# Performance work log

Measured on AMD Instinct MI355X. Metric: run time of the kernel, lower is better.

Reference implementation:

```python
import jax, jax.numpy as jnp
import numpy as np

B, S, D = 2, 2048, 2048
H, KVH = 32, 8
HD = D // H            # 64
G = H // KVH           # 4 kv groups
SCALE = 1.0 / np.sqrt(HD)


def setup_inputs() -> dict:
    key = jax.random.key(0)
    k1, k2, k3, k4, k5 = jax.random.split(key, 5)
    hidden_states = jax.random.normal(k1, (B, S, D), dtype=jnp.float32)
    Wq = jax.random.normal(k2, (D, H * HD), dtype=jnp.float32) * 0.02
    Wk = jax.random.normal(k3, (D, KVH * HD), dtype=jnp.float32) * 0.02
    Wv = jax.random.normal(k4, (D, KVH * HD), dtype=jnp.float32) * 0.02
    Wo = jax.random.normal(k5, (H * HD, D), dtype=jnp.float32) * 0.02
    return {"hidden_states": hidden_states, "Wq": Wq, "Wk": Wk, "Wv": Wv, "Wo": Wo}


def reference(hidden_states, Wq, Wk, Wv, Wo):
    B_, S_, _ = hidden_states.shape
    q = (hidden_states @ Wq).reshape(B_, S_, H, HD).transpose(0, 2, 1, 3)      # [B,H,S,HD]
    k = (hidden_states @ Wk).reshape(B_, S_, KVH, HD).transpose(0, 2, 1, 3)    # [B,KVH,S,HD]
    v = (hidden_states @ Wv).reshape(B_, S_, KVH, HD).transpose(0, 2, 1, 3)
    # repeat_interleave over head dim: kv head g serves q heads [g*G, (g+1)*G)
    k = jnp.repeat(k, G, axis=1)  # [B,H,S,HD]
    v = jnp.repeat(v, G, axis=1)
    scores = jnp.einsum('bhqd,bhkd->bhqk', q, k) * SCALE
    probs = jax.nn.softmax(scores.astype(jnp.float32), axis=-1).astype(q.dtype)
    # dropout is identity in eval mode
    out = jnp.einsum('bhqk,bhkd->bhqd', probs, v)             # [B,H,S,HD]
    out = out.transpose(0, 2, 1, 3).reshape(B_, S_, H * HD)   # [B,S,D]
    return out @ Wo
```

## Files before the change

kernel.cpp:

```cpp
#include <hip/hip_runtime.h>
#include <hip/hip_bf16.h>

typedef unsigned short u16;
typedef __attribute__((ext_vector_type(8))) short short8;
typedef __attribute__((ext_vector_type(4))) float f32x4;
typedef __attribute__((ext_vector_type(4))) unsigned short u16x4;

#define S_LEN 2048
#define NH 32
#define NKV 8
#define QSCALE 0.18033688011112042f
#define PSHIFT 14.0f

__device__ __forceinline__ float fexp2(float x) { return __builtin_amdgcn_exp2f(x); }

__device__ __forceinline__ u16 f2bf(float f) {
  unsigned int u = __builtin_bit_cast(unsigned int, f);
  u += 0x7fffu + ((u >> 16) & 1u);
  return (u16)(u >> 16);
}

__device__ __forceinline__ unsigned int pk2bf(float a, float b) {
  float2 t; t.x = a; t.y = b;
  __hip_bfloat162 h = __float22bfloat162_rn(t);
  unsigned int r;
  __builtin_memcpy(&r, &h, 4);
  return r;
}

__device__ __forceinline__ void async16(const void* g, void* l) {
  __builtin_amdgcn_global_load_lds(
      (__attribute__((address_space(1))) void*)g,
      (__attribute__((address_space(3))) void*)l, 16, 0, 0);
}

__global__ __launch_bounds__(256) void prep_kernel(const float* __restrict__ X,
                                                   const float* __restrict__ Wq,
                                                   const float* __restrict__ Wk,
                                                   const float* __restrict__ Wv,
                                                   const float* __restrict__ Wo,
                                                   u16* __restrict__ Xb,
                                                   u16* __restrict__ Wqt,
                                                   u16* __restrict__ Wkt,
                                                   u16* __restrict__ Wvt,
                                                   u16* __restrict__ Wot) {
  __shared__ float tile[32][33];
  int bx = blockIdx.x, tid = threadIdx.x;
  if (bx < 8192) {
    int idx = bx * 256 + tid;
    float4 v = ((const float4*)X)[idx];
    u16x4 o;
    o.x = f2bf(v.x); o.y = f2bf(v.y); o.z = f2bf(v.z); o.w = f2bf(v.w);
    *(u16x4*)&Xb[(size_t)idx * 4] = o;
    return;
  }
  const float* in; u16* out; int N, bi;
  if (bx < 12288)      { bi = bx - 8192;  in = Wq; out = Wqt; N = 2048; }
  else if (bx < 13312) { bi = bx - 12288; in = Wk; out = Wkt; N = 512; }
  else if (bx < 14336) { bi = bx - 13312; in = Wv; out = Wvt; N = 512; }
  else                 { bi = bx - 14336; in = Wo; out = Wot; N = 2048; }
  const int K = 2048;
  int nbx = N >> 5;
  int n0 = (bi % nbx) * 32, k0 = (bi / nbx) * 32;
  int tx = tid & 31, ty = tid >> 5;
#pragma unroll
  for (int i = 0; i < 32; i += 8)
    tile[ty + i][tx] = in[(size_t)(k0 + ty + i) * N + n0 + tx];
  __syncthreads();
#pragma unroll
  for (int i = 0; i < 32; i += 8)
    out[(size_t)(n0 + ty + i) * K + k0 + tx] = f2bf(tile[tx][ty + i]);
}

__global__ __launch_bounds__(256) void gemm_qkv(const u16* __restrict__ A,
                                                const u16* __restrict__ Wqt,
                                                const u16* __restrict__ Wkvt,
                                                u16* __restrict__ Qb,
                                                u16* __restrict__ KVb) {
  __shared__ u16 lds_a[128 * 32];
  __shared__ u16 lds_b[128 * 32];
  int tid = threadIdx.x, bx = blockIdx.x;
  int mode, bm, bn;
  const u16* Bt;
  if (bx < 512) { mode = 0; bm = bx >> 4; bn = bx & 15; Bt = Wqt; }
  else          { mode = 1; int b2 = bx - 512; bm = b2 >> 3; bn = b2 & 7; Bt = Wkvt; }
  const int K = 2048;
  int w = tid >> 6, lane = tid & 63, qd = lane >> 4, ln = lane & 15;
  int wm = w >> 1, wn = w & 1;
  const f32x4 z4 = {0.f, 0.f, 0.f, 0.f};
  f32x4 acc[4][4];
#pragma unroll
  for (int i = 0; i < 4; ++i)
#pragma unroll
    for (int j = 0; j < 4; ++j) acc[i][j] = z4;

  const u16* Ab = A + (size_t)bm * 128 * K;
  const u16* Bb = Bt + (size_t)bn * 128 * K;
  int row0 = tid >> 2, c0 = tid & 3;
  int g0 = c0 ^ (row0 & 3) ^ ((row0 >> 2) & 3);
  int s1 = tid + 256, row1 = s1 >> 2, c1 = s1 & 3;
  int g1 = c1 ^ (row1 & 3) ^ ((row1 >> 2) & 3);
  int pat = (ln & 3) ^ ((ln >> 2) & 3);
  int goff = (qd ^ pat) * 8;

  for (int kt = 0; kt < K; kt += 32) {
    async16(Ab + (size_t)row0 * K + kt + g0 * 8, &lds_a[tid * 8]);
    async16(Ab + (size_t)row1 * K + kt + g1 * 8, &lds_a[2048 + tid * 8]);
    async16(Bb + (size_t)row0 * K + kt + g0 * 8, &lds_b[tid * 8]);
    async16(Bb + (size_t)row1 * K + kt + g1 * 8, &lds_b[2048 + tid * 8]);
    __syncthreads();
    short8 af[4], bf[4];
#pragma unroll
    for (int i = 0; i < 4; ++i)
      af[i] = *(const short8*)&lds_a[(wm * 64 + i * 16 + ln) * 32 + goff];
#pragma unroll
    for (int j = 0; j < 4; ++j)
      bf[j] = *(const short8*)&lds_b[(wn * 64 + j * 16 + ln) * 32 + goff];
#pragma unroll
    for (int i = 0; i < 4; ++i)
#pragma unroll
      for (int j = 0; j < 4; ++j)
        acc[i][j] = __builtin_amdgcn_mfma_f32_16x16x32_bf16(af[i], bf[j], acc[i][j], 0, 0, 0);
    __syncthreads();
  }

#pragma unroll
  for (int i = 0; i < 4; ++i)
#pragma unroll
    for (int r = 0; r < 4; ++r) {
      int m = bm * 128 + wm * 64 + i * 16 + qd * 4 + r;
      int b = m >> 11, s = m & 2047;
#pragma unroll
      for (int j = 0; j < 4; ++j) {
        int n = bn * 128 + wn * 64 + j * 16 + ln;
        float v = acc[i][j][r];
        int hh = n >> 6, hd = n & 63;
        if (mode == 0) {
          Qb[(((size_t)(b * NH + hh)) * S_LEN + s) * 64 + hd] = f2bf(v * QSCALE);
        } else {
          if (hh < 8)
            KVb[(((size_t)(b * NKV + hh)) * S_LEN + s) * 64 + hd] = f2bf(v);
          else
            KVb[2097152 + (((size_t)(b * NKV + (hh - 8))) * 64 + hd) * S_LEN + s] = f2bf(v);
        }
      }
    }
}

__global__ __launch_bounds__(256) void gemm_out(const u16* __restrict__ A,
                                                const u16* __restrict__ Bt,
                                                float* __restrict__ outp) {
  __shared__ u16 lds_a[128 * 32];
  __shared__ u16 lds_b[128 * 32];
  const int K = 2048, N = 2048;
  int tid = threadIdx.x;
  int bm = blockIdx.x >> 4, bn = blockIdx.x & 15;
  int w = tid >> 6, lane = tid & 63, qd = lane >> 4, ln = lane & 15;
  int wm = w >> 1, wn = w & 1;
  const f32x4 z4 = {0.f, 0.f, 0.f, 0.f};
  f32x4 acc[4][4];
#pragma unroll
  for (int i = 0; i < 4; ++i)
#pragma unroll
    for (int j = 0; j < 4; ++j) acc[i][j] = z4;

  const u16* Ab = A + (size_t)bm * 128 * K;
  const u16* Bb = Bt + (size_t)bn * 128 * K;
  int row0 = tid >> 2, c0 = tid & 3;
  int g0 = c0 ^ (row0 & 3) ^ ((row0 >> 2) & 3);
  int s1 = tid + 256, row1 = s1 >> 2, c1 = s1 & 3;
  int g1 = c1 ^ (row1 & 3) ^ ((row1 >> 2) & 3);
  int pat = (ln & 3) ^ ((ln >> 2) & 3);
  int goff = (qd ^ pat) * 8;

  for (int kt = 0; kt < K; kt += 32) {
    async16(Ab + (size_t)row0 * K + kt + g0 * 8, &lds_a[tid * 8]);
    async16(Ab + (size_t)row1 * K + kt + g1 * 8, &lds_a[2048 + tid * 8]);
    async16(Bb + (size_t)row0 * K + kt + g0 * 8, &lds_b[tid * 8]);
    async16(Bb + (size_t)row1 * K + kt + g1 * 8, &lds_b[2048 + tid * 8]);
    __syncthreads();
    short8 af[4], bf[4];
#pragma unroll
    for (int i = 0; i < 4; ++i)
      af[i] = *(const short8*)&lds_a[(wm * 64 + i * 16 + ln) * 32 + goff];
#pragma unroll
    for (int j = 0; j < 4; ++j)
      bf[j] = *(const short8*)&lds_b[(wn * 64 + j * 16 + ln) * 32 + goff];
#pragma unroll
    for (int i = 0; i < 4; ++i)
#pragma unroll
      for (int j = 0; j < 4; ++j)
        acc[i][j] = __builtin_amdgcn_mfma_f32_16x16x32_bf16(af[i], bf[j], acc[i][j], 0, 0, 0);
    __syncthreads();
  }

#pragma unroll
  for (int i = 0; i < 4; ++i)
#pragma unroll
    for (int r = 0; r < 4; ++r) {
      int m = bm * 128 + wm * 64 + i * 16 + qd * 4 + r;
#pragma unroll
      for (int j = 0; j < 4; ++j) {
        int n = bn * 128 + wn * 64 + j * 16 + ln;
        outp[(size_t)m * N + n] = acc[i][j][r];
      }
    }
}

__global__ __launch_bounds__(256) void attn_kernel(const u16* __restrict__ Q,
                                                   const u16* __restrict__ K,
                                                   const u16* __restrict__ VT,
                                                   u16* __restrict__ Ao) {
  __shared__ u16 lds_k[2][4096];
  __shared__ u16 lds_v[2][4096];
  __shared__ u16 lds_p[4096];
  int tid = threadIdx.x;
  int w = tid >> 6, lane = tid & 63, qd = lane >> 4, ln = lane & 15;
  int qt = blockIdx.x & 15, bh = blockIdx.x >> 4;
  int b = bh >> 5, h = bh & 31, g = h >> 2;
  const u16* gQ = Q + ((size_t)bh * S_LEN + qt * 128) * 64;
  const u16* gK = K + (size_t)(b * NKV + g) * S_LEN * 64;
  const u16* gV = VT + (size_t)(b * NKV + g) * 64 * S_LEN;

  int pat7 = ln & 7;
  int sQ = (ln >> 1) & 3;
  int pw = w * 1024;

  int s0 = tid, r0 = s0 >> 3, c0 = s0 & 7, gg0 = c0 ^ (r0 & 7);
  int s1 = tid + 256, r1 = s1 >> 3, c1 = s1 & 7, gg1 = c1 ^ (r1 & 7);

  u16* qstage = &lds_k[0][0];
#pragma unroll
  for (int k = 0; k < 4; ++k) {
    int s = tid + k * 256;
    int q = s >> 3, c = s & 7, gg = c ^ (q & 7);
    async16(gQ + (size_t)q * 64 + gg * 8, &qstage[s * 8]);
  }
  __syncthreads();
  short8 qf[2][2];
#pragma unroll
  for (int i = 0; i < 2; ++i)
#pragma unroll
    for (int kc = 0; kc < 2; ++kc)
      qf[i][kc] = *(const short8*)&qstage[(w * 32 + i * 16 + ln) * 64 +
                                          ((kc * 4 + qd) ^ pat7) * 8];
  __syncthreads();

  async16(gK + (size_t)(r0)*64 + gg0 * 8, &lds_k[0][s0 * 8]);
  async16(gK + (size_t)(r1)*64 + gg1 * 8, &lds_k[0][s1 * 8]);
  async16(gV + (size_t)r0 * S_LEN + gg0 * 8, &lds_v[0][s0 * 8]);
  async16(gV + (size_t)r1 * S_LEN + gg1 * 8, &lds_v[0][s1 * 8]);
  __syncthreads();

  const f32x4 psh4 = {-PSHIFT, -PSHIFT, -PSHIFT, -PSHIFT};
  f32x4 accO[2][4];
  float li[2] = {0.f, 0.f};
#pragma unroll
  for (int i = 0; i < 2; ++i)
#pragma unroll
    for (int jn = 0; jn < 4; ++jn) accO[i][jn] = {0.f, 0.f, 0.f, 0.f};

  for (int c = 0; c < 32; ++c) {
    int cur = c & 1;
    if (c < 31) {
      int nb = cur ^ 1, cn = c + 1;
      async16(gK + (size_t)(cn * 64 + r0) * 64 + gg0 * 8, &lds_k[nb][s0 * 8]);
      async16(gK + (size_t)(cn * 64 + r1) * 64 + gg1 * 8, &lds_k[nb][s1 * 8]);
      async16(gV + (size_t)r0 * S_LEN + cn * 64 + gg0 * 8, &lds_v[nb][s0 * 8]);
      async16(gV + (size_t)r1 * S_LEN + cn * 64 + gg1 * 8, &lds_v[nb][s1 * 8]);
    }
    const u16* kb = lds_k[cur];
    const u16* vb = lds_v[cur];

    f32x4 sc[2][4];
    __builtin_amdgcn_s_setprio(1);
#pragma unroll
    for (int j = 0; j < 4; ++j) {
      short8 kf0 = *(const short8*)&kb[(j * 16 + ln) * 64 + ((0 + qd) ^ pat7) * 8];
      short8 kf1 = *(const short8*)&kb[(j * 16 + ln) * 64 + ((4 + qd) ^ pat7) * 8];
#pragma unroll
      for (int i = 0; i < 2; ++i) {
        sc[i][j] = __builtin_amdgcn_mfma_f32_16x16x32_bf16(kf0, qf[i][0], psh4, 0, 0, 0);
        sc[i][j] = __builtin_amdgcn_mfma_f32_16x16x32_bf16(kf1, qf[i][1], sc[i][j], 0, 0, 0);
      }
    }
    __builtin_amdgcn_s_setprio(0);

#pragma unroll
    for (int ph = 0; ph < 2; ++ph) {
#pragma unroll
      for (int i = 0; i < 2; ++i)
#pragma unroll
        for (int jj = 0; jj < 2; ++jj) {
          int j = ph * 2 + jj;
          float p0 = fexp2(sc[i][j][0]);
          float p1 = fexp2(sc[i][j][1]);
          float p2 = fexp2(sc[i][j][2]);
          float p3 = fexp2(sc[i][j][3]);
          li[i] += (p0 + p1) + (p2 + p3);
          uint2 pk;
          pk.x = pk2bf(p0, p1);
          pk.y = pk2bf(p2, p3);
          int pg = jj * 2 + (qd >> 1);
          *(uint2*)&lds_p[pw + (i * 16 + ln) * 32 + ((pg ^ sQ) * 8 + (qd & 1) * 4)] = pk;
        }
      short8 pf0 = *(const short8*)&lds_p[pw + ln * 32 + (qd ^ sQ) * 8];
      short8 pf1 = *(const short8*)&lds_p[pw + (16 + ln) * 32 + (qd ^ sQ) * 8];
      __builtin_amdgcn_s_setprio(1);
#pragma unroll
      for (int jn = 0; jn < 4; ++jn) {
        short8 vf = *(const short8*)&vb[(jn * 16 + ln) * 64 +
                                        (((ph * 4 + qd) ^ pat7) * 8)];
        accO[0][jn] = __builtin_amdgcn_mfma_f32_16x16x32_bf16(vf, pf0, accO[0][jn], 0, 0, 0);
        accO[1][jn] = __builtin_amdgcn_mfma_f32_16x16x32_bf16(vf, pf1, accO[1][jn], 0, 0, 0);
      }
      __builtin_amdgcn_s_setprio(0);
    }
    __syncthreads();
  }

#pragma unroll
  for (int i = 0; i < 2; ++i) {
    float l = li[i];
    l += __shfl_xor(l, 16);
    l += __shfl_xor(l, 32);
    float inv = 1.f / l;
    int q = qt * 128 + w * 32 + i * 16 + ln;
    size_t base = ((size_t)b * S_LEN + q) * 2048 + h * 64;
#pragma unroll
    for (int jn = 0; jn < 4; ++jn) {
      u16x4 o;
#pragma unroll
      for (int r = 0; r < 4; ++r) o[r] = f2bf(accO[i][jn][r] * inv);
      *(u16x4*)&Ao[base + jn * 16 + qd * 4] = o;
    }
  }
}

extern "C" void kernel_launch(void* const* d_in, const int* in_sizes, int n_in,
                              void* d_out, int out_size, void* d_ws, size_t ws_size,
                              hipStream_t stream) {
  const float* X  = (const float*)d_in[0];
  const float* Wq = (const float*)d_in[1];
  const float* Wk = (const float*)d_in[2];
  const float* Wv = (const float*)d_in[3];
  const float* Wo = (const float*)d_in[4];
  char* ws = (char*)d_ws;
  u16* Xb  = (u16*)(ws);
  u16* Wqt = (u16*)(ws + 16777216);
  u16* Wkt = (u16*)(ws + 25165824);
  u16* Wvt = (u16*)(ws + 27262976);
  u16* Wot = (u16*)(ws + 29360128);
  u16* Qb  = (u16*)(ws + 37748736);
  u16* Kb  = (u16*)(ws + 54525952);
  u16* VTb = (u16*)(ws + 58720256);
  u16* Ab  = (u16*)(ws + 62914560);
  float* out = (float*)d_out;

  prep_kernel<<<18432, 256, 0, stream>>>(X, Wq, Wk, Wv, Wo, Xb, Wqt, Wkt, Wvt, Wot);
  gemm_qkv<<<768, 256, 0, stream>>>(Xb, Wqt, Wkt, Qb, Kb);
  attn_kernel<<<1024, 256, 0, stream>>>(Qb, Kb, VTb, Ab);
  gemm_out<<<512, 256, 0, stream>>>(Ab, Wot, out);
}
```

Baseline: 331.4 us.

## Switch attention to 32x32x16 MFMA and pass P through permlane32 swaps

The attention kernel now computes the QK^T and PV products with 32x32x16 bf16 MFMA tiles instead of 16x16x32. The probability fragment is rearranged in registers with permlane32_swap instead of a round trip through shared memory, so the lds_p buffer is removed. The aim is to cut LDS traffic, fragment loads and MFMA issue count per chunk. In exchange, each lane holds larger 16-float accumulators, which raises register pressure. The post-prefetch sync before the loop is also removed, which relies on the in-loop barrier for ordering.

```diff
diff --git a/kernel.cpp b/kernel.cpp
--- a/kernel.cpp
+++ b/kernel.cpp
@@ -4,7 +4,9 @@
 typedef unsigned short u16;
 typedef __attribute__((ext_vector_type(8))) short short8;
 typedef __attribute__((ext_vector_type(4))) float f32x4;
+typedef __attribute__((ext_vector_type(16))) float f32x16;
 typedef __attribute__((ext_vector_type(4))) unsigned short u16x4;
+typedef __attribute__((ext_vector_type(4))) int int4v;
 
 #define S_LEN 2048
 #define NH 32
@@ -32,6 +34,11 @@
   __builtin_amdgcn_global_load_lds(
       (__attribute__((address_space(1))) void*)g,
       (__attribute__((address_space(3))) void*)l, 16, 0, 0);
+}
+
+__device__ __forceinline__ short8 mk_pf(unsigned a, unsigned b, unsigned c, unsigned d) {
+  int4v t; t.x = (int)a; t.y = (int)b; t.z = (int)c; t.w = (int)d;
+  return __builtin_bit_cast(short8, t);
 }
 
 __global__ __launch_bounds__(256) void prep_kernel(const float* __restrict__ X,
@@ -213,18 +220,16 @@
                                                    u16* __restrict__ Ao) {
   __shared__ u16 lds_k[2][4096];
   __shared__ u16 lds_v[2][4096];
-  __shared__ u16 lds_p[4096];
   int tid = threadIdx.x;
-  int w = tid >> 6, lane = tid & 63, qd = lane >> 4, ln = lane & 15;
+  int w = tid >> 6, lane = tid & 63;
+  int l31 = lane & 31, l5 = lane >> 5;
   int qt = blockIdx.x & 15, bh = blockIdx.x >> 4;
   int b = bh >> 5, h = bh & 31, g = h >> 2;
   const u16* gQ = Q + ((size_t)bh * S_LEN + qt * 128) * 64;
   const u16* gK = K + (size_t)(b * NKV + g) * S_LEN * 64;
   const u16* gV = VT + (size_t)(b * NKV + g) * 64 * S_LEN;
 
-  int pat7 = ln & 7;
-  int sQ = (ln >> 1) & 3;
-  int pw = w * 1024;
+  int p7 = l31 & 7;
 
   int s0 = tid, r0 = s0 >> 3, c0 = s0 & 7, gg0 = c0 ^ (r0 & 7);
   int s1 = tid + 256, r1 = s1 >> 3, c1 = s1 & 7, gg1 = c1 ^ (r1 & 7);
@@ -237,28 +242,27 @@
     async16(gQ + (size_t)q * 64 + gg * 8, &qstage[s * 8]);
   }
   __syncthreads();
-  short8 qf[2][2];
-#pragma unroll
-  for (int i = 0; i < 2; ++i)
-#pragma unroll
-    for (int kc = 0; kc < 2; ++kc)
-      qf[i][kc] = *(const short8*)&qstage[(w * 32 + i * 16 + ln) * 64 +
-                                          ((kc * 4 + qd) ^ pat7) * 8];
+  short8 qf[4];
+  int qrow = w * 32 + l31;
+#pragma unroll
+  for (int ks = 0; ks < 4; ++ks)
+    qf[ks] = *(const short8*)&qstage[qrow * 64 + ((ks * 2 + l5) ^ p7) * 8];
   __syncthreads();
 
-  async16(gK + (size_t)(r0)*64 + gg0 * 8, &lds_k[0][s0 * 8]);
-  async16(gK + (size_t)(r1)*64 + gg1 * 8, &lds_k[0][s1 * 8]);
+  async16(gK + (size_t)r0 * 64 + gg0 * 8, &lds_k[0][s0 * 8]);
+  async16(gK + (size_t)r1 * 64 + gg1 * 8, &lds_k[0][s1 * 8]);
   async16(gV + (size_t)r0 * S_LEN + gg0 * 8, &lds_v[0][s0 * 8]);
   async16(gV + (size_t)r1 * S_LEN + gg1 * 8, &lds_v[0][s1 * 8]);
-  __syncthreads();
-
-  const f32x4 psh4 = {-PSHIFT, -PSHIFT, -PSHIFT, -PSHIFT};
-  f32x4 accO[2][4];
-  float li[2] = {0.f, 0.f};
-#pragma unroll
-  for (int i = 0; i < 2; ++i)
-#pragma unroll
-    for (int jn = 0; jn < 4; ++jn) accO[i][jn] = {0.f, 0.f, 0.f, 0.f};
+
+  const f32x16 psh16 = {-PSHIFT, -PSHIFT, -PSHIFT, -PSHIFT, -PSHIFT, -PSHIFT,
+                        -PSHIFT, -PSHIFT, -PSHIFT, -PSHIFT, -PSHIFT, -PSHIFT,
+                        -PSHIFT, -PSHIFT, -PSHIFT, -PSHIFT};
+  f32x16 accO[2];
+#pragma unroll
+  for (int hb = 0; hb < 2; ++hb)
+#pragma unroll
+    for (int t = 0; t < 16; ++t) accO[hb][t] = 0.f;
+  float li = 0.f;
 
   for (int c = 0; c < 32; ++c) {
     int cur = c & 1;
@@ -272,69 +276,61 @@
     const u16* kb = lds_k[cur];
     const u16* vb = lds_v[cur];
 
-    f32x4 sc[2][4];
-    __builtin_amdgcn_s_setprio(1);
-#pragma unroll
-    for (int j = 0; j < 4; ++j) {
-      short8 kf0 = *(const short8*)&kb[(j * 16 + ln) * 64 + ((0 + qd) ^ pat7) * 8];
-      short8 kf1 = *(const short8*)&kb[(j * 16 + ln) * 64 + ((4 + qd) ^ pat7) * 8];
-#pragma unroll
-      for (int i = 0; i < 2; ++i) {
-        sc[i][j] = __builtin_amdgcn_mfma_f32_16x16x32_bf16(kf0, qf[i][0], psh4, 0, 0, 0);
-        sc[i][j] = __builtin_amdgcn_mfma_f32_16x16x32_bf16(kf1, qf[i][1], sc[i][j], 0, 0, 0);
-      }
-    }
-    __builtin_amdgcn_s_setprio(0);
-
-#pragma unroll
-    for (int ph = 0; ph < 2; ++ph) {
-#pragma unroll
-      for (int i = 0; i < 2; ++i)
-#pragma unroll
-        for (int jj = 0; jj < 2; ++jj) {
-          int j = ph * 2 + jj;
-          float p0 = fexp2(sc[i][j][0]);
-          float p1 = fexp2(sc[i][j][1]);
-          float p2 = fexp2(sc[i][j][2]);
-          float p3 = fexp2(sc[i][j][3]);
-          li[i] += (p0 + p1) + (p2 + p3);
-          uint2 pk;
-          pk.x = pk2bf(p0, p1);
-          pk.y = pk2bf(p2, p3);
-          int pg = jj * 2 + (qd >> 1);
-          *(uint2*)&lds_p[pw + (i * 16 + ln) * 32 + ((pg ^ sQ) * 8 + (qd & 1) * 4)] = pk;
-        }
-      short8 pf0 = *(const short8*)&lds_p[pw + ln * 32 + (qd ^ sQ) * 8];
-      short8 pf1 = *(const short8*)&lds_p[pw + (16 + ln) * 32 + (qd ^ sQ) * 8];
+#pragma unroll
+    for (int kblk = 0; kblk < 2; ++kblk) {
+      f32x16 sc = psh16;
       __builtin_amdgcn_s_setprio(1);
 #pragma unroll
-      for (int jn = 0; jn < 4; ++jn) {
-        short8 vf = *(const short8*)&vb[(jn * 16 + ln) * 64 +
-                                        (((ph * 4 + qd) ^ pat7) * 8)];
-        accO[0][jn] = __builtin_amdgcn_mfma_f32_16x16x32_bf16(vf, pf0, accO[0][jn], 0, 0, 0);
-        accO[1][jn] = __builtin_amdgcn_mfma_f32_16x16x32_bf16(vf, pf1, accO[1][jn], 0, 0, 0);
+      for (int ks = 0; ks < 4; ++ks) {
+        short8 kf = *(const short8*)&kb[(kblk * 32 + l31) * 64 + ((ks * 2 + l5) ^ p7) * 8];
+        sc = __builtin_amdgcn_mfma_f32_32x32x16_bf16(kf, qf[ks], sc, 0, 0, 0);
       }
       __builtin_amdgcn_s_setprio(0);
-    }
-    __syncthreads();
-  }
-
-#pragma unroll
-  for (int i = 0; i < 2; ++i) {
-    float l = li[i];
-    l += __shfl_xor(l, 16);
-    l += __shfl_xor(l, 32);
-    float inv = 1.f / l;
-    int q = qt * 128 + w * 32 + i * 16 + ln;
-    size_t base = ((size_t)b * S_LEN + q) * 2048 + h * 64;
-#pragma unroll
-    for (int jn = 0; jn < 4; ++jn) {
+
+      float p[16];
+#pragma unroll
+      for (int t = 0; t < 16; ++t) p[t] = fexp2(sc[t]);
+#pragma unroll
+      for (int t = 0; t < 16; t += 4) li += (p[t] + p[t + 1]) + (p[t + 2] + p[t + 3]);
+      unsigned W[8];
+#pragma unroll
+      for (int t = 0; t < 8; ++t) W[t] = pk2bf(p[2 * t], p[2 * t + 1]);
+      auto ra = __builtin_amdgcn_permlane32_swap((int)W[0], (int)W[2], false, false);
+      auto rb = __builtin_amdgcn_permlane32_swap((int)W[1], (int)W[3], false, false);
+      auto rc = __builtin_amdgcn_permlane32_swap((int)W[4], (int)W[6], false, false);
+      auto rd = __builtin_amdgcn_permlane32_swap((int)W[5], (int)W[7], false, false);
+      short8 pf0 = mk_pf((unsigned)ra[0], (unsigned)rb[0], (unsigned)ra[1], (unsigned)rb[1]);
+      short8 pf1 = mk_pf((unsigned)rc[0], (unsigned)rd[0], (unsigned)rc[1], (unsigned)rd[1]);
+
+      __builtin_amdgcn_s_setprio(1);
+#pragma unroll
+      for (int hb = 0; hb < 2; ++hb) {
+        short8 vf = *(const short8*)&vb[(hb * 32 + l31) * 64 + ((kblk * 4 + l5) ^ p7) * 8];
+        accO[hb] = __builtin_amdgcn_mfma_f32_32x32x16_bf16(vf, pf0, accO[hb], 0, 0, 0);
+      }
+#pragma unroll
+      for (int hb = 0; hb < 2; ++hb) {
+        short8 vf = *(const short8*)&vb[(hb * 32 + l31) * 64 + ((kblk * 4 + 2 + l5) ^ p7) * 8];
+        accO[hb] = __builtin_amdgcn_mfma_f32_32x32x16_bf16(vf, pf1, accO[hb], 0, 0, 0);
+      }
+      __builtin_amdgcn_s_setprio(0);
+    }
+    __syncthreads();
+  }
+
+  float l = li + __shfl_xor(li, 32);
+  float inv = 1.f / l;
+  int q = qt * 128 + w * 32 + l31;
+  size_t base = ((size_t)b * S_LEN + q) * 2048 + h * 64;
+#pragma unroll
+  for (int hb = 0; hb < 2; ++hb)
+#pragma unroll
+    for (int rq = 0; rq < 4; ++rq) {
       u16x4 o;
 #pragma unroll
-      for (int r = 0; r < 4; ++r) o[r] = f2bf(accO[i][jn][r] * inv);
-      *(u16x4*)&Ao[base + jn * 16 + qd * 4] = o;
-    }
-  }
+      for (int rr = 0; rr < 4; ++rr) o[rr] = f2bf(accO[hb][rq * 4 + rr] * inv);
+      *(u16x4*)&Ao[base + hb * 32 + rq * 8 + l5 * 4] = o;
+    }
 }
 
 extern "C" void kernel_launch(void* const* d_in, const int* in_sizes, int n_in,
```

Measured after the change: 331.5 us. Within noise of the previous version (+0.0%).
